# Performance work log

Hardware: AMD Instinct MI355X
Metric: run time of the kernel (lower is better)

Reference implementation:

```python
import jax, jax.numpy as jnp
import numpy as np

B, N_HM, K_APP, S = 16, 32, 16, 256

def setup_inputs() -> dict:
    key = jax.random.key(0)
    k1, k2, k3 = jax.random.split(key, 3)
    # x: post-UNet appearance feature map [B, K, S, S]
    x = jax.random.normal(k1, (B, K_APP, S, S), dtype=jnp.float32)
    # raw_tps: raw heatmap logits [B, N, S, S]
    raw_tps = jax.random.normal(k2, (B, N_HM, S, S), dtype=jnp.float32)
    # fitted_cj: non-negative fitted heatmaps [B, N, S, S]
    fitted_cj = jax.random.uniform(k3, (B, N_HM, S, S), dtype=jnp.float32)
    return {"x": x, "raw_tps": raw_tps, "fitted_cj": fitted_cj}

def reference(x, raw_tps, fitted_cj):
    # torch F.softmax on a 2D [S,S] tensor with no dim defaults to dim=1 -> per-row softmax
    p = jax.nn.softmax(raw_tps, axis=-1)                      # [B, N, S, S]
    # attention pooling: app_vec[b,n,k] = sum_{h,w} x[b,k,h,w] * p[b,n,h,w]
    app_vec = jnp.einsum('bkhw,bnhw->bnk', x, p)              # [B, N, K]
    # weighted combine without materializing the [B,N,S,S,K] repeat
    num = jnp.einsum('bnhw,bnk->bhwk', fitted_cj, app_vec)    # [B, S, S, K]
    denom = 1.0 + jnp.sum(fitted_cj, axis=1)[..., None]       # [B, S, S, 1]
    app_enco = num / denom                                     # [B, S, S, K]
    # transpose(2,3) then transpose(1,2): [B,S,S,K] -> [B,K,S,S]
    return jnp.transpose(app_enco, (0, 3, 1, 2))
```

## Files before the change

### kernel.cpp

```cpp
#include <hip/hip_runtime.h>

#define S_DIM 256
#define N_HM 32
#define K_APP 16
#define HW (S_DIM * S_DIM)
#define LDS_PAD 260

template <bool ATOMIC>
__global__ __launch_bounds__(256) void k1_softmax_pool(
    const float* __restrict__ x,
    const float* __restrict__ raw,
    float* __restrict__ outp)
{
    __shared__ float p_lds[N_HM][LDS_PAD];
    __shared__ float x_lds[K_APP][LDS_PAD];

    const int tid  = threadIdx.x;
    const int b    = blockIdx.x >> 8;
    const int h    = blockIdx.x & 255;
    const int wid  = tid >> 6;
    const int lane = tid & 63;

    {
        const int c4 = lane;
        const float* basep = raw + ((size_t)(b * N_HM) << 16) + (h << 8);
        #pragma unroll
        for (int it = 0; it < 8; ++it) {
            int n = it * 4 + wid;
            float4 v = *(const float4*)(basep + ((size_t)n << 16) + (c4 << 2));
            *(float4*)&p_lds[n][c4 << 2] = v;
        }
        const float* basex = x + ((size_t)(b * K_APP) << 16) + (h << 8);
        #pragma unroll
        for (int it = 0; it < 4; ++it) {
            int k = it * 4 + wid;
            float4 v = *(const float4*)(basex + ((size_t)k << 16) + (c4 << 2));
            *(float4*)&x_lds[k][c4 << 2] = v;
        }
    }
    __syncthreads();

    #pragma unroll
    for (int i = 0; i < 8; ++i) {
        int n = wid * 8 + i;
        float4 v = *(const float4*)&p_lds[n][lane << 2];
        float m = fmaxf(fmaxf(v.x, v.y), fmaxf(v.z, v.w));
        #pragma unroll
        for (int off = 32; off > 0; off >>= 1) m = fmaxf(m, __shfl_xor(m, off));
        float e0 = __expf(v.x - m), e1 = __expf(v.y - m);
        float e2 = __expf(v.z - m), e3 = __expf(v.w - m);
        float s = e0 + e1 + e2 + e3;
        #pragma unroll
        for (int off = 32; off > 0; off >>= 1) s += __shfl_xor(s, off);
        float inv = 1.0f / s;
        *(float4*)&p_lds[n][lane << 2] = make_float4(e0 * inv, e1 * inv, e2 * inv, e3 * inv);
    }
    __syncthreads();

    const int wt = (tid >> 3) & 7;
    const int c  = tid & 7;
    const int n0 = (((wid >> 1) * 4) + (wt & 3)) * 4;
    const int k0 = (((wid & 1) * 2) + (wt >> 2)) * 4;

    float acc[4][4];
    #pragma unroll
    for (int i = 0; i < 4; ++i)
        #pragma unroll
        for (int j = 0; j < 4; ++j) acc[i][j] = 0.0f;

    #pragma unroll
    for (int j = 0; j < 8; ++j) {
        const int w = (c << 2) + (j << 5);
        float4 pv[4], xv[4];
        #pragma unroll
        for (int i = 0; i < 4; ++i) pv[i] = *(const float4*)&p_lds[n0 + i][w];
        #pragma unroll
        for (int i = 0; i < 4; ++i) xv[i] = *(const float4*)&x_lds[k0 + i][w];
        #pragma unroll
        for (int i = 0; i < 4; ++i)
            #pragma unroll
            for (int jj = 0; jj < 4; ++jj)
                acc[i][jj] += pv[i].x * xv[jj].x + pv[i].y * xv[jj].y +
                              pv[i].z * xv[jj].z + pv[i].w * xv[jj].w;
    }

    #pragma unroll
    for (int off = 4; off > 0; off >>= 1)
        #pragma unroll
        for (int i = 0; i < 4; ++i)
            #pragma unroll
            for (int jj = 0; jj < 4; ++jj)
                acc[i][jj] += __shfl_down(acc[i][jj], off, 8);

    if (c == 0) {
        if (ATOMIC) {
            float* av = outp + (b << 9);
            #pragma unroll
            for (int i = 0; i < 4; ++i)
                #pragma unroll
                for (int jj = 0; jj < 4; ++jj)
                    atomicAdd(&av[(n0 + i) * 16 + k0 + jj], acc[i][jj]);
        } else {
            float* dst = outp + ((size_t)blockIdx.x << 9);
            #pragma unroll
            for (int i = 0; i < 4; ++i)
                *(float4*)(dst + (n0 + i) * 16 + k0) =
                    make_float4(acc[i][0], acc[i][1], acc[i][2], acc[i][3]);
        }
    }
}

__global__ __launch_bounds__(256) void k1_reduce(
    const float* __restrict__ partial, float* __restrict__ av)
{
    const int gid = blockIdx.x * 256 + threadIdx.x;
    const int b = gid >> 9;
    const int r = gid & 511;
    const float* p = partial + ((size_t)(b << 8) << 9) + r;
    float s = 0.0f;
    #pragma unroll 8
    for (int h = 0; h < 256; ++h) s += p[(size_t)h << 9];
    av[gid] = s;
}

__global__ __launch_bounds__(256) void k2_combine(
    const float* __restrict__ fit,
    const float* __restrict__ av,
    float* __restrict__ out)
{
    const int tid = threadIdx.x;
    const int b   = blockIdx.x >> 8;
    const int hw  = ((blockIdx.x & 255) << 8) + tid;

    const float* avb = av + (b << 9);
    const float* fb  = fit + ((size_t)(b * N_HM) << 16) + hw;

    float num[16];
    #pragma unroll
    for (int k = 0; k < 16; ++k) num[k] = 0.0f;
    float den = 1.0f;

    #pragma unroll 4
    for (int n = 0; n < 32; ++n) {
        float f = fb[(size_t)n << 16];
        den += f;
        const float4* ar = (const float4*)(avb + (n << 4));
        float4 a0 = ar[0], a1 = ar[1], a2 = ar[2], a3 = ar[3];
        num[0]  += f * a0.x;  num[1]  += f * a0.y;  num[2]  += f * a0.z;  num[3]  += f * a0.w;
        num[4]  += f * a1.x;  num[5]  += f * a1.y;  num[6]  += f * a1.z;  num[7]  += f * a1.w;
        num[8]  += f * a2.x;  num[9]  += f * a2.y;  num[10] += f * a2.z;  num[11] += f * a2.w;
        num[12] += f * a3.x;  num[13] += f * a3.y;  num[14] += f * a3.z;  num[15] += f * a3.w;
    }

    const float inv = 1.0f / den;
    float* ob = out + ((size_t)(b * K_APP) << 16) + hw;
    #pragma unroll
    for (int k = 0; k < 16; ++k) ob[(size_t)k << 16] = num[k] * inv;
}

extern "C" void kernel_launch(void* const* d_in, const int* in_sizes, int n_in,
                              void* d_out, int out_size, void* d_ws, size_t ws_size,
                              hipStream_t stream)
{
    const float* x   = (const float*)d_in[0];
    const float* raw = (const float*)d_in[1];
    const float* fit = (const float*)d_in[2];
    float* out = (float*)d_out;

    float* av      = (float*)d_ws;
    float* partial = (float*)d_ws + 8192;
    const size_t need = (size_t)(8192 + 4096 * 512) * sizeof(float);

    const int nblk = 16 * S_DIM;

    if (ws_size >= need) {
        k1_softmax_pool<false><<<nblk, 256, 0, stream>>>(x, raw, partial);
        k1_reduce<<<8192 / 256, 256, 0, stream>>>(partial, av);
    } else {
        hipMemsetAsync(av, 0, 8192 * sizeof(float), stream);
        k1_softmax_pool<true><<<nblk, 256, 0, stream>>>(x, raw, av);
    }
    k2_combine<<<nblk, 256, 0, stream>>>(fit, av, out);
}
```

Measured before the change: 347.2 us.

## Register-resident softmax-pool, parallelize partial reduce, float2 combine kernel

The softmax-pool kernel drops its LDS staging and keeps each row's x values in registers, prefetching the next heatmap row while the current one is processed. It then does a transpose-style butterfly shuffle so 16 lanes end up holding the 16 k-sums. The reduce kernel now splits the 256-row sum across 8 thread groups combined through LDS, which gives more blocks and more memory parallelism. The combine kernel processes two pixels per thread with float2 loads and stores, halving the grid. The main risk is register pressure from 16 float4 plus accumulators under the new launch bounds.

```diff
diff --git a/kernel.cpp b/kernel.cpp
--- a/kernel.cpp
+++ b/kernel.cpp
@@ -4,108 +4,84 @@
 #define N_HM 32
 #define K_APP 16
 #define HW (S_DIM * S_DIM)
-#define LDS_PAD 260
 
 template <bool ATOMIC>
-__global__ __launch_bounds__(256) void k1_softmax_pool(
+__global__ __launch_bounds__(256, 4) void k1_softmax_pool(
     const float* __restrict__ x,
     const float* __restrict__ raw,
     float* __restrict__ outp)
 {
-    __shared__ float p_lds[N_HM][LDS_PAD];
-    __shared__ float x_lds[K_APP][LDS_PAD];
-
     const int tid  = threadIdx.x;
     const int b    = blockIdx.x >> 8;
     const int h    = blockIdx.x & 255;
     const int wid  = tid >> 6;
     const int lane = tid & 63;
 
-    {
-        const int c4 = lane;
-        const float* basep = raw + ((size_t)(b * N_HM) << 16) + (h << 8);
-        #pragma unroll
-        for (int it = 0; it < 8; ++it) {
-            int n = it * 4 + wid;
-            float4 v = *(const float4*)(basep + ((size_t)n << 16) + (c4 << 2));
-            *(float4*)&p_lds[n][c4 << 2] = v;
-        }
-        const float* basex = x + ((size_t)(b * K_APP) << 16) + (h << 8);
-        #pragma unroll
-        for (int it = 0; it < 4; ++it) {
-            int k = it * 4 + wid;
-            float4 v = *(const float4*)(basex + ((size_t)k << 16) + (c4 << 2));
-            *(float4*)&x_lds[k][c4 << 2] = v;
-        }
-    }
-    __syncthreads();
+    const float* xb = x + ((size_t)(b * K_APP) << 16) + (h << 8) + (lane << 2);
+    float4 xv[K_APP];
+    #pragma unroll
+    for (int k = 0; k < K_APP; ++k)
+        xv[k] = *(const float4*)(xb + ((size_t)k << 16));
+
+    const float* rb = raw + ((size_t)(b * N_HM) << 16) + (h << 8) + (lane << 2);
+
+    float4 nxt = *(const float4*)(rb + ((size_t)(wid * 8) << 16));
 
     #pragma unroll
     for (int i = 0; i < 8; ++i) {
-        int n = wid * 8 + i;
-        float4 v = *(const float4*)&p_lds[n][lane << 2];
-        float m = fmaxf(fmaxf(v.x, v.y), fmaxf(v.z, v.w));
+        const int n = wid * 8 + i;
+        float4 cur = nxt;
+        if (i < 7) nxt = *(const float4*)(rb + ((size_t)(n + 1) << 16));
+
+        float m = fmaxf(fmaxf(cur.x, cur.y), fmaxf(cur.z, cur.w));
         #pragma unroll
         for (int off = 32; off > 0; off >>= 1) m = fmaxf(m, __shfl_xor(m, off));
-        float e0 = __expf(v.x - m), e1 = __expf(v.y - m);
-        float e2 = __expf(v.z - m), e3 = __expf(v.w - m);
+        float e0 = __expf(cur.x - m), e1 = __expf(cur.y - m);
+        float e2 = __expf(cur.z - m), e3 = __expf(cur.w - m);
         float s = e0 + e1 + e2 + e3;
         #pragma unroll
         for (int off = 32; off > 0; off >>= 1) s += __shfl_xor(s, off);
-        float inv = 1.0f / s;
-        *(float4*)&p_lds[n][lane << 2] = make_float4(e0 * inv, e1 * inv, e2 * inv, e3 * inv);
-    }
-    __syncthreads();
+        const float inv = 1.0f / s;
 
-    const int wt = (tid >> 3) & 7;
-    const int c  = tid & 7;
-    const int n0 = (((wid >> 1) * 4) + (wt & 3)) * 4;
-    const int k0 = (((wid & 1) * 2) + (wt >> 2)) * 4;
+        float A[16];
+        #pragma unroll
+        for (int k = 0; k < K_APP; ++k)
+            A[k] = e0 * xv[k].x + e1 * xv[k].y + e2 * xv[k].z + e3 * xv[k].w;
 
-    float acc[4][4];
-    #pragma unroll
-    for (int i = 0; i < 4; ++i)
         #pragma unroll
-        for (int j = 0; j < 4; ++j) acc[i][j] = 0.0f;
+        for (int j = 0; j < 8; ++j) {
+            float send = (lane & 8) ? A[j] : A[j + 8];
+            float keep = (lane & 8) ? A[j + 8] : A[j];
+            A[j] = keep + __shfl_xor(send, 8);
+        }
+        #pragma unroll
+        for (int j = 0; j < 4; ++j) {
+            float send = (lane & 4) ? A[j] : A[j + 4];
+            float keep = (lane & 4) ? A[j + 4] : A[j];
+            A[j] = keep + __shfl_xor(send, 4);
+        }
+        #pragma unroll
+        for (int j = 0; j < 2; ++j) {
+            float send = (lane & 2) ? A[j] : A[j + 2];
+            float keep = (lane & 2) ? A[j + 2] : A[j];
+            A[j] = keep + __shfl_xor(send, 2);
+        }
+        {
+            float send = (lane & 1) ? A[0] : A[1];
+            float keep = (lane & 1) ? A[1] : A[0];
+            A[0] = keep + __shfl_xor(send, 1);
+        }
+        float v = A[0];
+        v += __shfl_xor(v, 16);
+        v += __shfl_xor(v, 32);
+        v *= inv;
 
-    #pragma unroll
-    for (int j = 0; j < 8; ++j) {
-        const int w = (c << 2) + (j << 5);
-        float4 pv[4], xv[4];
-        #pragma unroll
-        for (int i = 0; i < 4; ++i) pv[i] = *(const float4*)&p_lds[n0 + i][w];
-        #pragma unroll
-        for (int i = 0; i < 4; ++i) xv[i] = *(const float4*)&x_lds[k0 + i][w];
-        #pragma unroll
-        for (int i = 0; i < 4; ++i)
-            #pragma unroll
-            for (int jj = 0; jj < 4; ++jj)
-                acc[i][jj] += pv[i].x * xv[jj].x + pv[i].y * xv[jj].y +
-                              pv[i].z * xv[jj].z + pv[i].w * xv[jj].w;
-    }
-
-    #pragma unroll
-    for (int off = 4; off > 0; off >>= 1)
-        #pragma unroll
-        for (int i = 0; i < 4; ++i)
-            #pragma unroll
-            for (int jj = 0; jj < 4; ++jj)
-                acc[i][jj] += __shfl_down(acc[i][jj], off, 8);
-
-    if (c == 0) {
         if (ATOMIC) {
-            float* av = outp + (b << 9);
-            #pragma unroll
-            for (int i = 0; i < 4; ++i)
-                #pragma unroll
-                for (int jj = 0; jj < 4; ++jj)
-                    atomicAdd(&av[(n0 + i) * 16 + k0 + jj], acc[i][jj]);
+            if (lane < 16)
+                atomicAdd(outp + (b << 9) + (n << 4) + lane, v);
         } else {
-            float* dst = outp + ((size_t)blockIdx.x << 9);
-            #pragma unroll
-            for (int i = 0; i < 4; ++i)
-                *(float4*)(dst + (n0 + i) * 16 + k0) =
-                    make_float4(acc[i][0], acc[i][1], acc[i][2], acc[i][3]);
+            if (lane < 16)
+                outp[((size_t)blockIdx.x << 9) + (n << 4) + lane] = v;
         }
     }
 }
@@ -113,49 +89,74 @@
 __global__ __launch_bounds__(256) void k1_reduce(
     const float* __restrict__ partial, float* __restrict__ av)
 {
-    const int gid = blockIdx.x * 256 + threadIdx.x;
-    const int b = gid >> 9;
-    const int r = gid & 511;
-    const float* p = partial + ((size_t)(b << 8) << 9) + r;
+    __shared__ float s_lds[256];
+    const int tid = threadIdx.x;
+    const int o   = (blockIdx.x << 5) + (tid & 31);
+    const int ch  = tid >> 5;
+    const int b   = o >> 9;
+    const int r   = o & 511;
+
+    const float* p = partial + ((size_t)((b << 8) + (ch << 5)) << 9) + r;
     float s = 0.0f;
     #pragma unroll 8
-    for (int h = 0; h < 256; ++h) s += p[(size_t)h << 9];
-    av[gid] = s;
+    for (int j = 0; j < 32; ++j) s += p[(size_t)j << 9];
+
+    s_lds[tid] = s;
+    __syncthreads();
+    if (tid < 32) {
+        float t = s_lds[tid];
+        #pragma unroll
+        for (int c = 1; c < 8; ++c) t += s_lds[tid + (c << 5)];
+        av[o] = t;
+    }
 }
 
-__global__ __launch_bounds__(256) void k2_combine(
+__global__ __launch_bounds__(256, 4) void k2_combine(
     const float* __restrict__ fit,
     const float* __restrict__ av,
     float* __restrict__ out)
 {
     const int tid = threadIdx.x;
-    const int b   = blockIdx.x >> 8;
-    const int hw  = ((blockIdx.x & 255) << 8) + tid;
+    const int b   = blockIdx.x >> 7;
+    const int hw2 = ((blockIdx.x & 127) << 8) + tid;
 
-    const float* avb = av + (b << 9);
-    const float* fb  = fit + ((size_t)(b * N_HM) << 16) + hw;
+    const float*  avb = av + (b << 9);
+    const float2* fb  = (const float2*)fit + ((size_t)(b * N_HM) << 15) + hw2;
 
-    float num[16];
+    float2 num[16];
     #pragma unroll
-    for (int k = 0; k < 16; ++k) num[k] = 0.0f;
-    float den = 1.0f;
+    for (int k = 0; k < 16; ++k) num[k] = make_float2(0.0f, 0.0f);
+    float dx = 1.0f, dy = 1.0f;
 
-    #pragma unroll 4
-    for (int n = 0; n < 32; ++n) {
-        float f = fb[(size_t)n << 16];
-        den += f;
+    #pragma unroll 8
+    for (int n = 0; n < N_HM; ++n) {
+        float2 f = fb[(size_t)n << 15];
+        dx += f.x; dy += f.y;
         const float4* ar = (const float4*)(avb + (n << 4));
         float4 a0 = ar[0], a1 = ar[1], a2 = ar[2], a3 = ar[3];
-        num[0]  += f * a0.x;  num[1]  += f * a0.y;  num[2]  += f * a0.z;  num[3]  += f * a0.w;
-        num[4]  += f * a1.x;  num[5]  += f * a1.y;  num[6]  += f * a1.z;  num[7]  += f * a1.w;
-        num[8]  += f * a2.x;  num[9]  += f * a2.y;  num[10] += f * a2.z;  num[11] += f * a2.w;
-        num[12] += f * a3.x;  num[13] += f * a3.y;  num[14] += f * a3.z;  num[15] += f * a3.w;
+        num[0].x  += f.x * a0.x;  num[0].y  += f.y * a0.x;
+        num[1].x  += f.x * a0.y;  num[1].y  += f.y * a0.y;
+        num[2].x  += f.x * a0.z;  num[2].y  += f.y * a0.z;
+        num[3].x  += f.x * a0.w;  num[3].y  += f.y * a0.w;
+        num[4].x  += f.x * a1.x;  num[4].y  += f.y * a1.x;
+        num[5].x  += f.x * a1.y;  num[5].y  += f.y * a1.y;
+        num[6].x  += f.x * a1.z;  num[6].y  += f.y * a1.z;
+        num[7].x  += f.x * a1.w;  num[7].y  += f.y * a1.w;
+        num[8].x  += f.x * a2.x;  num[8].y  += f.y * a2.x;
+        num[9].x  += f.x * a2.y;  num[9].y  += f.y * a2.y;
+        num[10].x += f.x * a2.z;  num[10].y += f.y * a2.z;
+        num[11].x += f.x * a2.w;  num[11].y += f.y * a2.w;
+        num[12].x += f.x * a3.x;  num[12].y += f.y * a3.x;
+        num[13].x += f.x * a3.y;  num[13].y += f.y * a3.y;
+        num[14].x += f.x * a3.z;  num[14].y += f.y * a3.z;
+        num[15].x += f.x * a3.w;  num[15].y += f.y * a3.w;
     }
 
-    const float inv = 1.0f / den;
-    float* ob = out + ((size_t)(b * K_APP) << 16) + hw;
+    const float ix = 1.0f / dx, iy = 1.0f / dy;
+    float2* ob = (float2*)out + ((size_t)(b * K_APP) << 15) + hw2;
     #pragma unroll
-    for (int k = 0; k < 16; ++k) ob[(size_t)k << 16] = num[k] * inv;
+    for (int k = 0; k < 16; ++k)
+        ob[(size_t)k << 15] = make_float2(num[k].x * ix, num[k].y * iy);
 }
 
 extern "C" void kernel_launch(void* const* d_in, const int* in_sizes, int n_in,
@@ -171,14 +172,12 @@
     float* partial = (float*)d_ws + 8192;
     const size_t need = (size_t)(8192 + 4096 * 512) * sizeof(float);
 
-    const int nblk = 16 * S_DIM;
-
     if (ws_size >= need) {
-        k1_softmax_pool<false><<<nblk, 256, 0, stream>>>(x, raw, partial);
-        k1_reduce<<<8192 / 256, 256, 0, stream>>>(partial, av);
+        k1_softmax_pool<false><<<4096, 256, 0, stream>>>(x, raw, partial);
+        k1_reduce<<<256, 256, 0, stream>>>(partial, av);
     } else {
         hipMemsetAsync(av, 0, 8192 * sizeof(float), stream);
-        k1_softmax_pool<true><<<nblk, 256, 0, stream>>>(x, raw, av);
+        k1_softmax_pool<true><<<4096, 256, 0, stream>>>(x, raw, av);
     }
-    k2_combine<<<nblk, 256, 0, stream>>>(fit, av, out);
+    k2_combine<<<2048, 256, 0, stream>>>(fit, av, out);
 }
```

Measured after the change: 341.4 us. About the same (-1.7%).
